# Performance work log

Measured on AMD Instinct MI355X. Metric: run time of the kernel, lower is better.

Reference implementation:

```python
import jax, jax.numpy as jnp
import numpy as np

H = 256      # hidden_dim
NH = 4       # num_heads
DK = H // NH # per-head dim
NL = 2       # num self-attn layers
TL = 6       # transformer_num_layers (output repeat)
PTS_DIM = 3


def _layer_norm(x, g, b, eps=1e-5):
    m = jnp.mean(x, axis=-1, keepdims=True)
    v = jnp.mean((x - m) ** 2, axis=-1, keepdims=True)
    return (x - m) / jnp.sqrt(v + eps) * g + b


def _mha(x, Wq, bq, Wk, bk, Wv, bv, Wo, bo, g, bb, bias):
    # x: [B,N,H]; bias: [B,NH,N,N]; way='add' (att_spm_type='add')
    B, N, _ = x.shape
    q = (x @ Wq + bq).reshape(B, N, NH, DK).transpose(0, 2, 1, 3)  # [B,h,N,d]
    k = (x @ Wk + bk).reshape(B, N, NH, DK).transpose(0, 2, 1, 3)
    v = (x @ Wv + bv).reshape(B, N, NH, DK).transpose(0, 2, 1, 3)
    att = jnp.einsum('bhnd,bhmd->bhnm', q, k) / np.sqrt(DK).astype(np.float32)
    att = jax.nn.softmax(att + bias, axis=-1)
    out = jnp.einsum('bhnm,bhmd->bhnd', att, v).transpose(0, 2, 1, 3).reshape(B, N, H)
    out = out @ Wo + bo
    return _layer_norm(x + out, g, bb)


def setup_inputs() -> dict:
    key = jax.random.key(0)
    ks = jax.random.split(key, 16)
    B, N = 1, 512
    s = 0.02  # weight init scale
    inp = {
        'history_states': jax.random.normal(ks[0], (TL, B, N, H), jnp.float32),
        'all_lanes_preds': jax.random.normal(ks[1], (TL, B, N, 33), jnp.float32),
        'fc_W': jax.random.normal(ks[2], (H, H), jnp.float32) * s,
        'fc_b': jnp.zeros((H,), jnp.float32),
        'Wq': jax.random.normal(ks[3], (NL, H, H), jnp.float32) * s,
        'bq': jnp.zeros((NL, H), jnp.float32),
        'Wk': jax.random.normal(ks[4], (NL, H, H), jnp.float32) * s,
        'bk': jnp.zeros((NL, H), jnp.float32),
        'Wv': jax.random.normal(ks[5], (NL, H, H), jnp.float32) * s,
        'bv': jnp.zeros((NL, H), jnp.float32),
        'Wo': jax.random.normal(ks[6], (NL, H, H), jnp.float32) * s,
        'bo': jnp.zeros((NL, H), jnp.float32),
        'ln_g': jnp.ones((NL, H), jnp.float32),
        'ln_b': jnp.zeros((NL, H), jnp.float32),
        'mlp1_W': jax.random.normal(ks[7], (H, H), jnp.float32) * s,
        'mlp1_b': jnp.zeros((H,), jnp.float32),
        'mlp2_W': jax.random.normal(ks[8], (H, H), jnp.float32) * s,
        'mlp2_b': jnp.zeros((H,), jnp.float32),
        'cls_W1': jax.random.normal(ks[9], (2 * H, H), jnp.float32) * s,
        'cls_b1': jnp.zeros((H,), jnp.float32),
        'cls_W2': jax.random.normal(ks[10], (H, 1), jnp.float32) * s,
        'cls_b2': jnp.zeros((1,), jnp.float32),
    }
    return inp


def reference(history_states, all_lanes_preds, fc_W, fc_b, Wq, bq, Wk, bk, Wv, bv,
              Wo, bo, ln_g, ln_b, mlp1_W, mlp1_b, mlp2_W, mlp2_b,
              cls_W1, cls_b1, cls_W2, cls_b2):
    query_feats = history_states[-1]                 # [B,N,H]
    coords = all_lanes_preds[-1]                      # [B,N,33]
    B, N, C = coords.shape
    coords = coords.reshape(B, N, C // PTS_DIM, PTS_DIM)
    query_end_point = coords[:, :, -1, :]             # [B,N,3]
    key_start_point = coords[:, :, 0, :]              # [B,N,3]

    # pairwise distance bias: dist[b,i,j] = ||key_start[j] - query_end[i]||
    diff = key_start_point[:, None, :, :] - query_end_point[:, :, None, :]
    dist = jnp.sqrt(jnp.sum(diff ** 2, axis=-1))[:, None, :, :]  # [B,1,N,N]
    dw = 1.0 / (dist + 0.01)
    dw = dw / jnp.sum(dw, axis=2, keepdims=True)      # normalize over dim 2
    zeros = jnp.zeros_like(dw)
    dist_weights = jax.lax.stop_gradient(
        jnp.concatenate([dw, -dist, zeros, zeros], axis=1))  # [B,4,N,N]

    # features_concat: Linear + ReLU
    x = jax.nn.relu(query_feats @ fc_W + fc_b)

    for i in range(NL):
        x = _mha(x, Wq[i], bq[i], Wk[i], bk[i], Wv[i], bv[i],
                 Wo[i], bo[i], ln_g[i], ln_b[i], dist_weights)

    # lclc relationship head: per-side MLP, pairwise concat, classifier
    o1 = jax.nn.relu(x @ mlp1_W + mlp1_b)             # [B,N,H]
    o2 = jax.nn.relu(x @ mlp2_W + mlp2_b)
    pair = jnp.concatenate([
        jnp.broadcast_to(o1[:, :, None, :], (B, N, N, H)),
        jnp.broadcast_to(o2[:, None, :, :], (B, N, N, H))], axis=-1)  # [B,N,N,2H]
    z = jax.nn.relu(pair @ cls_W1 + cls_b1)
    lclc = (z @ cls_W2 + cls_b2)[..., 0]              # [B,N,N]
    all_lclc_preds = jnp.broadcast_to(lclc[None], (TL, B, N, N))
    return all_lclc_preds
```

## Files before the change

### kernel.cpp

```cpp
#include <hip/hip_runtime.h>
#include <math.h>


#define NTOK 512
#define HDIM 256
#define DKH  64
#define NHEAD 4
#define TLEN 6
#define WSZ  65536
#define PSTR 520

typedef __attribute__((ext_vector_type(8))) short bf16x8;
typedef __attribute__((ext_vector_type(4))) float f32x4;

__device__ __forceinline__ ushort f2bf(float f)
{
    unsigned u = __builtin_bit_cast(unsigned, f);
    u += 0x7FFFu + ((u >> 16) & 1u);
    return (ushort)(u >> 16);
}

struct PKArg {
    const float* w[13];
    const float* qf; const float* pl;
    ushort* wpk; ushort* qf16;
    float *dist, *dwraw, *inv_cs;
};

__global__ __launch_bounds__(256) void pack_kernel(PKArg p)
{
    __shared__ __align__(16) ushort smu[64 * 72];
    const int bid = blockIdx.x;
    const int t   = threadIdx.x;

    if (bid < 208) {
        const int mat  = bid >> 4;
        const int tile = bid & 15;
        const int k0   = (tile >> 2) * 64;
        const int c0   = (tile & 3) * 64;
        const float* W = p.w[mat];
#pragma unroll
        for (int j = 0; j < 4; ++j) {
            const int i  = t + j * 256;
            const int r  = i >> 4, c4 = i & 15;
            const float4 v4 = *(const float4*)&W[(k0 + r) * HDIM + c0 + c4 * 4];
            smu[(c4 * 4 + 0) * 72 + r] = f2bf(v4.x);
            smu[(c4 * 4 + 1) * 72 + r] = f2bf(v4.y);
            smu[(c4 * 4 + 2) * 72 + r] = f2bf(v4.z);
            smu[(c4 * 4 + 3) * 72 + r] = f2bf(v4.w);
        }
        __syncthreads();
#pragma unroll
        for (int j = 0; j < 2; ++j) {
            const int i  = t + j * 256;
            const int cr = i >> 3, kk = i & 7;
            const uint4 v = *(const uint4*)&smu[cr * 72 + kk * 8];
            *(uint4*)&p.wpk[mat * WSZ + (c0 + cr) * HDIM + k0 + kk * 8] = v;
        }
    } else if (bid < 224) {
        const int r0 = (bid - 208) * 32;
#pragma unroll
        for (int j = 0; j < 8; ++j) {
            const int i  = t + j * 256;
            const int r  = i >> 6, c4 = i & 63;
            const float4 v4 = *(const float4*)&p.qf[(r0 + r) * HDIM + c4 * 4];
            ushort4 s = {f2bf(v4.x), f2bf(v4.y), f2bf(v4.z), f2bf(v4.w)};
            *(ushort4*)&p.qf16[(r0 + r) * HDIM + c4 * 4] = s;
        }
    } else {
        float* smf = (float*)smu;
        float* qe  = smf;
        float* red = smf + 1536;
        const int item = bid - 224;
        for (int i = t; i < 512; i += 256) {
            qe[i * 3 + 0] = p.pl[i * 33 + 30];
            qe[i * 3 + 1] = p.pl[i * 33 + 31];
            qe[i * 3 + 2] = p.pl[i * 33 + 32];
        }
        __syncthreads();
        const int m   = item * 64 + (t & 63);
        const int nch = t >> 6;
        const float kx = p.pl[m * 33 + 0], ky = p.pl[m * 33 + 1], kz = p.pl[m * 33 + 2];
        float cs = 0.f;
        for (int n = nch * 128; n < nch * 128 + 128; ++n) {
            const float dx = kx - qe[n * 3 + 0];
            const float dy = ky - qe[n * 3 + 1];
            const float dz = kz - qe[n * 3 + 2];
            const float dd = sqrtf(dx * dx + dy * dy + dz * dz);
            const float w  = 1.0f / (dd + 0.01f);
            p.dist[n * NTOK + m]  = dd;
            p.dwraw[n * NTOK + m] = w;
            cs += w;
        }
        red[nch * 64 + (t & 63)] = cs;
        __syncthreads();
        if (t < 64)
            p.inv_cs[item * 64 + t] =
                1.0f / (red[t] + red[64 + t] + red[128 + t] + red[192 + t]);
    }
}

struct GB { const ushort* A16; const ushort* Wt; const float* b;
            float* C; ushort* C16; ushort* C16T; };

__global__ __launch_bounds__(256) void gemm_bf(GB g0, GB g1, GB g2, int relu)
{
    const int bid = blockIdx.x;
    const GB g = (bid < 64) ? g0 : (bid < 128) ? g1 : g2;
    const int t = threadIdx.x;
    const int wv = t >> 6, lane = t & 63;
    const int gw = (bid & 63) * 4 + wv;
    const int rg = gw >> 3, cg = gw & 7;
    const int lr = lane & 15, lg = lane >> 4, lk = lg * 8;

    const ushort* Arow = g.A16 + (rg * 16 + lr) * HDIM + lk;
    const ushort* Brow = g.Wt + (cg * 32 + lr) * HDIM + lk;

    f32x4 acc[2];
    acc[0] = (f32x4){0.f, 0.f, 0.f, 0.f};
    acc[1] = (f32x4){0.f, 0.f, 0.f, 0.f};

#pragma unroll
    for (int ks = 0; ks < 8; ++ks) {
        const bf16x8 a = *(const bf16x8*)&Arow[ks * 32];
#pragma unroll
        for (int j = 0; j < 2; ++j) {
            const bf16x8 b = *(const bf16x8*)&Brow[j * 16 * HDIM + ks * 32];
            acc[j] = __builtin_amdgcn_mfma_f32_16x16x32_bf16(a, b, acc[j], 0, 0, 0);
        }
    }

    const int orow = rg * 16 + lg * 4;
#pragma unroll
    for (int j = 0; j < 2; ++j) {
        const int col = cg * 32 + j * 16 + lr;
        const float bbv = g.b ? g.b[col] : 0.f;
        float o[4];
#pragma unroll
        for (int r = 0; r < 4; ++r) {
            o[r] = acc[j][r] + bbv;
            if (relu) o[r] = fmaxf(o[r], 0.f);
            if (g.C)   g.C[(orow + r) * HDIM + col] = o[r];
            if (g.C16) g.C16[(orow + r) * HDIM + col] = f2bf(o[r]);
        }
        if (g.C16T) {
            ushort4 s = {f2bf(o[0]), f2bf(o[1]), f2bf(o[2]), f2bf(o[3])};
            *(ushort4*)&g.C16T[col * NTOK + orow] = s;
        }
    }
}

__global__ __launch_bounds__(256) void attn_fused(
    const ushort* __restrict__ q16, const ushort* __restrict__ k16,
    const ushort* __restrict__ vT16, const float* __restrict__ dist,
    const float* __restrict__ dwraw, const float* __restrict__ inv_cs,
    ushort* __restrict__ ao16)
{
    __shared__ __align__(16) ushort P_lds[16 * PSTR];
    __shared__ __align__(16) float exch[4][16][64];
    __shared__ float rmax[4][16];
    __shared__ float psums[4][16];

    const int bid = blockIdx.x;
    const int h  = bid >> 5;
    const int n0 = (bid & 31) * 16;
    const int t  = threadIdx.x;
    const int wv = t >> 6, lane = t & 63;
    const int lr = lane & 15, lg = lane >> 4, lk = lg * 8;
    const int mW = wv * 128;

    const ushort* Qrow = q16 + (n0 + lr) * HDIM + h * DKH + lk;
    const bf16x8 a0 = *(const bf16x8*)&Qrow[0];
    const bf16x8 a1 = *(const bf16x8*)&Qrow[32];

    f32x4 accs[8];
#pragma unroll
    for (int cg = 0; cg < 8; ++cg) accs[cg] = (f32x4){0.f, 0.f, 0.f, 0.f};
#pragma unroll
    for (int cg = 0; cg < 8; ++cg) {
        const ushort* Brow = k16 + (mW + cg * 16 + lr) * HDIM + h * DKH + lk;
        accs[cg] = __builtin_amdgcn_mfma_f32_16x16x32_bf16(
            a0, *(const bf16x8*)&Brow[0], accs[cg], 0, 0, 0);
        accs[cg] = __builtin_amdgcn_mfma_f32_16x16x32_bf16(
            a1, *(const bf16x8*)&Brow[32], accs[cg], 0, 0, 0);
    }

    float s[8][4];
#pragma unroll
    for (int cg = 0; cg < 8; ++cg) {
        const int m = mW + cg * 16 + lr;
        const float ic = (h == 0) ? inv_cs[m] : 0.f;
#pragma unroll
        for (int rg = 0; rg < 4; ++rg) {
            const int n = n0 + lg * 4 + rg;
            float b = 0.f;
            if (h == 0)      b = dwraw[n * NTOK + m] * ic;
            else if (h == 1) b = -dist[n * NTOK + m];
            s[cg][rg] = accs[cg][rg] * 0.125f + b;
        }
    }

    float mx[4];
#pragma unroll
    for (int rg = 0; rg < 4; ++rg) {
        float m = s[0][rg];
#pragma unroll
        for (int cg = 1; cg < 8; ++cg) m = fmaxf(m, s[cg][rg]);
#pragma unroll
        for (int o = 1; o < 16; o <<= 1) m = fmaxf(m, __shfl_xor(m, o));
        mx[rg] = m;
    }
    if (lr == 0)
#pragma unroll
        for (int rg = 0; rg < 4; ++rg) rmax[wv][lg * 4 + rg] = mx[rg];
    __syncthreads();
    float mxf[4];
#pragma unroll
    for (int rg = 0; rg < 4; ++rg) {
        const int row = lg * 4 + rg;
        mxf[rg] = fmaxf(fmaxf(rmax[0][row], rmax[1][row]),
                        fmaxf(rmax[2][row], rmax[3][row]));
    }

    float ps[4] = {0.f, 0.f, 0.f, 0.f};
#pragma unroll
    for (int cg = 0; cg < 8; ++cg)
#pragma unroll
        for (int rg = 0; rg < 4; ++rg) {
            const float e = __expf(s[cg][rg] - mxf[rg]);
            ps[rg] += e;
            P_lds[(lg * 4 + rg) * PSTR + mW + cg * 16 + lr] = f2bf(e);
        }
#pragma unroll
    for (int rg = 0; rg < 4; ++rg) {
#pragma unroll
        for (int o = 1; o < 16; o <<= 1) ps[rg] += __shfl_xor(ps[rg], o);
    }
    if (lr == 0)
#pragma unroll
        for (int rg = 0; rg < 4; ++rg) psums[wv][lg * 4 + rg] = ps[rg];
    __syncthreads();

    f32x4 acco[4];
#pragma unroll
    for (int db = 0; db < 4; ++db) acco[db] = (f32x4){0.f, 0.f, 0.f, 0.f};
#pragma unroll
    for (int c = 0; c < 4; ++c) {
        const bf16x8 pa = *(const bf16x8*)&P_lds[lr * PSTR + mW + c * 32 + lk];
#pragma unroll
        for (int db = 0; db < 4; ++db) {
            const bf16x8 b = *(const bf16x8*)
                &vT16[(h * DKH + db * 16 + lr) * NTOK + mW + c * 32 + lk];
            acco[db] = __builtin_amdgcn_mfma_f32_16x16x32_bf16(pa, b, acco[db], 0, 0, 0);
        }
    }
#pragma unroll
    for (int db = 0; db < 4; ++db)
#pragma unroll
        for (int rg = 0; rg < 4; ++rg)
            exch[wv][lg * 4 + rg][db * 16 + lr] = acco[db][rg];
    __syncthreads();

    {
        const int r = t >> 4, d4 = t & 15;
        f32x4 sum = *(const f32x4*)&exch[0][r][d4 * 4];
        sum += *(const f32x4*)&exch[1][r][d4 * 4];
        sum += *(const f32x4*)&exch[2][r][d4 * 4];
        sum += *(const f32x4*)&exch[3][r][d4 * 4];
        const float inv = 1.0f / (psums[0][r] + psums[1][r] + psums[2][r] + psums[3][r]);
        ushort4 o = {f2bf(sum.x * inv), f2bf(sum.y * inv),
                     f2bf(sum.z * inv), f2bf(sum.w * inv)};
        *(ushort4*)&ao16[(n0 + r) * HDIM + h * DKH + d4 * 4] = o;
    }
}

__global__ __launch_bounds__(256) void oprojln(
    const ushort* __restrict__ ao16, const ushort* __restrict__ WoT,
    const float* __restrict__ bo, const float* __restrict__ g,
    const float* __restrict__ bb, float* __restrict__ x,
    ushort* __restrict__ x16)
{
    __shared__ float red[4][16];

    const int n0 = blockIdx.x * 16;
    const int t  = threadIdx.x;
    const int wv = t >> 6, lane = t & 63;
    const int lr = lane & 15, lg = lane >> 4, lk = lg * 8;

    const ushort* Arow = ao16 + (n0 + lr) * HDIM + lk;

    f32x4 acc[4];
#pragma unroll
    for (int j = 0; j < 4; ++j) acc[j] = (f32x4){0.f, 0.f, 0.f, 0.f};

#pragma unroll
    for (int ks = 0; ks < 8; ++ks) {
        const bf16x8 a = *(const bf16x8*)&Arow[ks * 32];
#pragma unroll
        for (int j = 0; j < 4; ++j) {
            const bf16x8 b = *(const bf16x8*)
                &WoT[(wv * 64 + j * 16 + lr) * HDIM + ks * 32 + lk];
            acc[j] = __builtin_amdgcn_mfma_f32_16x16x32_bf16(a, b, acc[j], 0, 0, 0);
        }
    }

#pragma unroll
    for (int j = 0; j < 4; ++j) {
        const int col = wv * 64 + j * 16 + lr;
        const float bc = bo[col];
#pragma unroll
        for (int rg = 0; rg < 4; ++rg)
            acc[j][rg] += bc + x[(n0 + lg * 4 + rg) * HDIM + col];
    }

    float sm[4];
#pragma unroll
    for (int rg = 0; rg < 4; ++rg) {
        float s = 0.f;
#pragma unroll
        for (int j = 0; j < 4; ++j) s += acc[j][rg];
#pragma unroll
        for (int o = 1; o < 16; o <<= 1) s += __shfl_xor(s, o);
        sm[rg] = s;
    }
    if (lr == 0)
#pragma unroll
        for (int rg = 0; rg < 4; ++rg) red[wv][lg * 4 + rg] = sm[rg];
    __syncthreads();
    float mean[4];
#pragma unroll
    for (int rg = 0; rg < 4; ++rg) {
        const int row = lg * 4 + rg;
        mean[rg] = (red[0][row] + red[1][row] + red[2][row] + red[3][row]) * (1.f / 256.f);
    }
    __syncthreads();

#pragma unroll
    for (int rg = 0; rg < 4; ++rg) {
        float s2 = 0.f;
#pragma unroll
        for (int j = 0; j < 4; ++j) {
            const float c = acc[j][rg] - mean[rg];
            s2 += c * c;
        }
#pragma unroll
        for (int o = 1; o < 16; o <<= 1) s2 += __shfl_xor(s2, o);
        sm[rg] = s2;
    }
    if (lr == 0)
#pragma unroll
        for (int rg = 0; rg < 4; ++rg) red[wv][lg * 4 + rg] = sm[rg];
    __syncthreads();
    float rstd[4];
#pragma unroll
    for (int rg = 0; rg < 4; ++rg) {
        const int row = lg * 4 + rg;
        const float var = (red[0][row] + red[1][row] + red[2][row] + red[3][row]) * (1.f / 256.f);
        rstd[rg] = rsqrtf(var + 1e-5f);
    }

#pragma unroll
    for (int j = 0; j < 4; ++j) {
        const int col = wv * 64 + j * 16 + lr;
        const float gg = g[col], bv = bb[col];
#pragma unroll
        for (int rg = 0; rg < 4; ++rg) {
            const int row = n0 + lg * 4 + rg;
            const float o = (acc[j][rg] - mean[rg]) * rstd[rg] * gg + bv;
            x[row * HDIM + col]   = o;
            x16[row * HDIM + col] = f2bf(o);
        }
    }
}

__global__ __launch_bounds__(256) void pair_cls(const float* __restrict__ U1,
                                                const float* __restrict__ U2,
                                                const float* __restrict__ W2,
                                                const float* __restrict__ b2,
                                                float* __restrict__ out)
{
    __shared__ __align__(16) float u1s[32][260];
    __shared__ __align__(16) float u2s[32][260];
    __shared__ __align__(16) float w2s[256];
    const int t  = threadIdx.x;
    const int n0 = blockIdx.y * 32, m0 = blockIdx.x * 32;

    for (int i = t; i < 32 * 64; i += 256) {
        const int r = i >> 6, c4 = i & 63;
        *(float4*)&u1s[r][c4 * 4] = *(const float4*)&U1[(n0 + r) * HDIM + c4 * 4];
        *(float4*)&u2s[r][c4 * 4] = *(const float4*)&U2[(m0 + r) * HDIM + c4 * 4];
    }
    if (t < 64) *(float4*)&w2s[t * 4] = *(const float4*)&W2[t * 4];
    __syncthreads();

    const int tx = t & 15, ty = t >> 4;
    float acc[2][2] = {};
    for (int h4 = 0; h4 < 64; ++h4) {
        const float4 a0 = *(const float4*)&u1s[ty * 2][h4 * 4];
        const float4 a1 = *(const float4*)&u1s[ty * 2 + 1][h4 * 4];
        const float4 b0 = *(const float4*)&u2s[tx * 2][h4 * 4];
        const float4 b1 = *(const float4*)&u2s[tx * 2 + 1][h4 * 4];
        const float4 w  = *(const float4*)&w2s[h4 * 4];
#define RT(A, B) fmaxf((A) + (B), 0.f)
        acc[0][0] += RT(a0.x,b0.x)*w.x + RT(a0.y,b0.y)*w.y + RT(a0.z,b0.z)*w.z + RT(a0.w,b0.w)*w.w;
        acc[0][1] += RT(a0.x,b1.x)*w.x + RT(a0.y,b1.y)*w.y + RT(a0.z,b1.z)*w.z + RT(a0.w,b1.w)*w.w;
        acc[1][0] += RT(a1.x,b0.x)*w.x + RT(a1.y,b0.y)*w.y + RT(a1.z,b0.z)*w.z + RT(a1.w,b0.w)*w.w;
        acc[1][1] += RT(a1.x,b1.x)*w.x + RT(a1.y,b1.y)*w.y + RT(a1.z,b1.z)*w.z + RT(a1.w,b1.w)*w.w;
#undef RT
    }
    const float bbv = b2[0];
#pragma unroll
    for (int ii = 0; ii < 2; ++ii)
#pragma unroll
        for (int jj = 0; jj < 2; ++jj) {
            const float val = acc[ii][jj] + bbv;
            const int n = n0 + ty * 2 + ii;
            const int m = m0 + tx * 2 + jj;
#pragma unroll
            for (int tl = 0; tl < TLEN; ++tl)
                out[tl * NTOK * NTOK + n * NTOK + m] = val;
        }
}

extern "C" void kernel_launch(void* const* d_in, const int* in_sizes, int n_in,
                              void* d_out, int out_size, void* d_ws, size_t ws_size,
                              hipStream_t stream)
{
    const float* hs   = (const float*)d_in[0];
    const float* qf   = hs + 5 * NTOK * HDIM;
    const float* alp  = (const float*)d_in[1];
    const float* pl   = alp + 5 * NTOK * 33;
    const float* fc_W = (const float*)d_in[2];
    const float* fc_b = (const float*)d_in[3];
    const float* Wq   = (const float*)d_in[4];
    const float* bq   = (const float*)d_in[5];
    const float* Wk   = (const float*)d_in[6];
    const float* bk   = (const float*)d_in[7];
    const float* Wv   = (const float*)d_in[8];
    const float* bv   = (const float*)d_in[9];
    const float* Wo   = (const float*)d_in[10];
    const float* bo   = (const float*)d_in[11];
    const float* lng  = (const float*)d_in[12];
    const float* lnb  = (const float*)d_in[13];
    const float* m1W  = (const float*)d_in[14];
    const float* m1b  = (const float*)d_in[15];
    const float* m2W  = (const float*)d_in[16];
    const float* m2b  = (const float*)d_in[17];
    const float* cW1  = (const float*)d_in[18];
    const float* cb1  = (const float*)d_in[19];
    const float* cW2  = (const float*)d_in[20];
    const float* cb2  = (const float*)d_in[21];
    float* out = (float*)d_out;

    const int NN  = NTOK * NTOK;
    const int NH_ = NTOK * HDIM;
    float* ws     = (float*)d_ws;
    float* dist   = ws;
    float* dwraw  = ws + NN;
    float* inv_cs = ws + 2 * NN;
    float* x      = ws + 2 * NN + 512;
    float* U1     = x + NH_;
    float* U2     = U1 + NH_;
    ushort* u16   = (ushort*)(U2 + NH_);
    ushort* wpk   = u16;
    ushort* qf16  = wpk + 13 * WSZ;
    ushort* x16   = qf16 + NH_;
    ushort* q16   = x16 + NH_;
    ushort* k16   = q16 + NH_;
    ushort* vT16  = k16 + NH_;
    ushort* ao16  = vT16 + NH_;
    ushort* o116  = ao16 + NH_;
    ushort* o216  = o116 + NH_;

    PKArg pk;
    pk.w[0]  = fc_W;
    pk.w[1]  = Wq;  pk.w[2]  = Wq + WSZ;
    pk.w[3]  = Wk;  pk.w[4]  = Wk + WSZ;
    pk.w[5]  = Wv;  pk.w[6]  = Wv + WSZ;
    pk.w[7]  = Wo;  pk.w[8]  = Wo + WSZ;
    pk.w[9]  = m1W; pk.w[10] = m2W;
    pk.w[11] = cW1; pk.w[12] = cW1 + WSZ;
    pk.qf = qf; pk.pl = pl;
    pk.wpk = wpk; pk.qf16 = qf16;
    pk.dist = dist; pk.dwraw = dwraw; pk.inv_cs = inv_cs;
    pack_kernel<<<232, 256, 0, stream>>>(pk);

    const GB gzb = {nullptr, nullptr, nullptr, nullptr, nullptr, nullptr};

    gemm_bf<<<64, 256, 0, stream>>>(
        GB{qf16, wpk + 0 * WSZ, fc_b, x, x16, nullptr}, gzb, gzb, 1);

    for (int L = 0; L < 2; ++L) {
        const ushort* wq = wpk + (1 + L) * WSZ;
        const ushort* wk = wpk + (3 + L) * WSZ;
        const ushort* wv = wpk + (5 + L) * WSZ;
        const ushort* wo = wpk + (7 + L) * WSZ;

        gemm_bf<<<192, 256, 0, stream>>>(
            GB{x16, wq, bq + L * HDIM, nullptr, q16, nullptr},
            GB{x16, wk, bk + L * HDIM, nullptr, k16, nullptr},
            GB{x16, wv, bv + L * HDIM, nullptr, nullptr, vT16}, 0);

        attn_fused<<<128, 256, 0, stream>>>(
            q16, k16, vT16, dist, dwraw, inv_cs, ao16);

        oprojln<<<32, 256, 0, stream>>>(
            ao16, wo, bo + L * HDIM, lng + L * HDIM, lnb + L * HDIM, x, x16);
    }

    gemm_bf<<<128, 256, 0, stream>>>(
        GB{x16, wpk + 9 * WSZ, m1b, nullptr, o116, nullptr},
        GB{x16, wpk + 10 * WSZ, m2b, nullptr, o216, nullptr}, gzb, 1);
    gemm_bf<<<128, 256, 0, stream>>>(
        GB{o116, wpk + 11 * WSZ, cb1, U1, nullptr, nullptr},
        GB{o216, wpk + 12 * WSZ, nullptr, U2, nullptr, nullptr}, gzb, 0);

    pair_cls<<<dim3(16, 16), 256, 0, stream>>>(U1, U2, cW2, cb2, out);
}
```

Baseline: 109.7 us.

## Fuse row-slab GEMM chains into fewer kernels with LDS-resident panels

Replaces the separate generic GEMM launches with fused per-16-row-slab kernels. These chain fc→QKV, oproj+LayerNorm→next-layer QKV, and oproj+LN→MLP1/MLP2→classifier-W1, keeping the intermediate activations in LDS panels. The fc input is now converted to bf16 inside the GEMM, so the separate conversion pass in the pack kernel goes away. Kernel launches drop from 10 to 7 and several global round-trips are removed. In exchange only 32 blocks run each fused GEMM stage, and each wave does more serial MFMA work, so parallelism per stage is lower.

Measured after the change: 153.2 us. +39.6%, slower.

```diff
diff --git a/kernel.cpp b/kernel.cpp
--- a/kernel.cpp
+++ b/kernel.cpp
@@ -9,6 +9,7 @@
 #define TLEN 6
 #define WSZ  65536
 #define PSTR 520
+#define XPS  264
 
 typedef __attribute__((ext_vector_type(8))) short bf16x8;
 typedef __attribute__((ext_vector_type(4))) float f32x4;
@@ -22,8 +23,8 @@
 
 struct PKArg {
     const float* w[13];
-    const float* qf; const float* pl;
-    ushort* wpk; ushort* qf16;
+    const float* pl;
+    ushort* wpk;
     float *dist, *dwraw, *inv_cs;
 };
 
@@ -57,21 +58,11 @@
             const uint4 v = *(const uint4*)&smu[cr * 72 + kk * 8];
             *(uint4*)&p.wpk[mat * WSZ + (c0 + cr) * HDIM + k0 + kk * 8] = v;
         }
-    } else if (bid < 224) {
-        const int r0 = (bid - 208) * 32;
-#pragma unroll
-        for (int j = 0; j < 8; ++j) {
-            const int i  = t + j * 256;
-            const int r  = i >> 6, c4 = i & 63;
-            const float4 v4 = *(const float4*)&p.qf[(r0 + r) * HDIM + c4 * 4];
-            ushort4 s = {f2bf(v4.x), f2bf(v4.y), f2bf(v4.z), f2bf(v4.w)};
-            *(ushort4*)&p.qf16[(r0 + r) * HDIM + c4 * 4] = s;
-        }
     } else {
         float* smf = (float*)smu;
         float* qe  = smf;
         float* red = smf + 1536;
-        const int item = bid - 224;
+        const int item = bid - 208;
         for (int i = t; i < 512; i += 256) {
             qe[i * 3 + 0] = p.pl[i * 33 + 30];
             qe[i * 3 + 1] = p.pl[i * 33 + 31];
@@ -100,54 +91,101 @@
     }
 }
 
-struct GB { const ushort* A16; const ushort* Wt; const float* b;
-            float* C; ushort* C16; ushort* C16T; };
-
-__global__ __launch_bounds__(256) void gemm_bf(GB g0, GB g1, GB g2, int relu)
-{
-    const int bid = blockIdx.x;
-    const GB g = (bid < 64) ? g0 : (bid < 128) ? g1 : g2;
+__device__ __forceinline__ void qkv_phase(
+    const ushort* __restrict__ xpan,
+    const ushort* __restrict__ WqT, const float* __restrict__ bq,
+    const ushort* __restrict__ WkT, const float* __restrict__ bk,
+    const ushort* __restrict__ WvT, const float* __restrict__ bv,
+    int slab, int c0, int lr, int lg, int lk,
+    ushort* __restrict__ q16, ushort* __restrict__ k16,
+    ushort* __restrict__ vT16)
+{
+    const ushort* Ap = xpan + lr * XPS + lk;
+#pragma unroll
+    for (int p = 0; p < 3; ++p) {
+        const ushort* Wt = (p == 0) ? WqT : (p == 1) ? WkT : WvT;
+        const float*  bb = (p == 0) ? bq  : (p == 1) ? bk  : bv;
+        f32x4 acc[4];
+#pragma unroll
+        for (int j = 0; j < 4; ++j) acc[j] = (f32x4){0.f, 0.f, 0.f, 0.f};
+#pragma unroll
+        for (int ks = 0; ks < 8; ++ks) {
+            const bf16x8 a = *(const bf16x8*)&Ap[ks * 32];
+#pragma unroll
+            for (int j = 0; j < 4; ++j) {
+                const bf16x8 b = *(const bf16x8*)&Wt[(c0 + j * 16 + lr) * HDIM + ks * 32 + lk];
+                acc[j] = __builtin_amdgcn_mfma_f32_16x16x32_bf16(a, b, acc[j], 0, 0, 0);
+            }
+        }
+#pragma unroll
+        for (int j = 0; j < 4; ++j) {
+            const int col = c0 + j * 16 + lr;
+            const float bv2 = bb[col];
+            if (p < 2) {
+                ushort* dst = (p == 0) ? q16 : k16;
+#pragma unroll
+                for (int rg = 0; rg < 4; ++rg)
+                    dst[(slab + lg * 4 + rg) * HDIM + col] = f2bf(acc[j][rg] + bv2);
+            } else {
+                ushort4 s = {f2bf(acc[j][0] + bv2), f2bf(acc[j][1] + bv2),
+                             f2bf(acc[j][2] + bv2), f2bf(acc[j][3] + bv2)};
+                *(ushort4*)&vT16[col * NTOK + slab + lg * 4] = s;
+            }
+        }
+    }
+}
+
+__global__ __launch_bounds__(256) void fcqkv(
+    const float* __restrict__ qf, const ushort* __restrict__ fcWt,
+    const float* __restrict__ fcb,
+    const ushort* __restrict__ WqT, const float* __restrict__ bq,
+    const ushort* __restrict__ WkT, const float* __restrict__ bk,
+    const ushort* __restrict__ WvT, const float* __restrict__ bv,
+    float* __restrict__ x, ushort* __restrict__ q16,
+    ushort* __restrict__ k16, ushort* __restrict__ vT16)
+{
+    __shared__ __align__(16) ushort xpan[16 * XPS];
+    const int slab = blockIdx.x * 16;
     const int t = threadIdx.x;
     const int wv = t >> 6, lane = t & 63;
-    const int gw = (bid & 63) * 4 + wv;
-    const int rg = gw >> 3, cg = gw & 7;
     const int lr = lane & 15, lg = lane >> 4, lk = lg * 8;
-
-    const ushort* Arow = g.A16 + (rg * 16 + lr) * HDIM + lk;
-    const ushort* Brow = g.Wt + (cg * 32 + lr) * HDIM + lk;
-
-    f32x4 acc[2];
-    acc[0] = (f32x4){0.f, 0.f, 0.f, 0.f};
-    acc[1] = (f32x4){0.f, 0.f, 0.f, 0.f};
-
-#pragma unroll
-    for (int ks = 0; ks < 8; ++ks) {
-        const bf16x8 a = *(const bf16x8*)&Arow[ks * 32];
-#pragma unroll
-        for (int j = 0; j < 2; ++j) {
-            const bf16x8 b = *(const bf16x8*)&Brow[j * 16 * HDIM + ks * 32];
-            acc[j] = __builtin_amdgcn_mfma_f32_16x16x32_bf16(a, b, acc[j], 0, 0, 0);
-        }
-    }
-
-    const int orow = rg * 16 + lg * 4;
-#pragma unroll
-    for (int j = 0; j < 2; ++j) {
-        const int col = cg * 32 + j * 16 + lr;
-        const float bbv = g.b ? g.b[col] : 0.f;
-        float o[4];
-#pragma unroll
-        for (int r = 0; r < 4; ++r) {
-            o[r] = acc[j][r] + bbv;
-            if (relu) o[r] = fmaxf(o[r], 0.f);
-            if (g.C)   g.C[(orow + r) * HDIM + col] = o[r];
-            if (g.C16) g.C16[(orow + r) * HDIM + col] = f2bf(o[r]);
-        }
-        if (g.C16T) {
-            ushort4 s = {f2bf(o[0]), f2bf(o[1]), f2bf(o[2]), f2bf(o[3])};
-            *(ushort4*)&g.C16T[col * NTOK + orow] = s;
-        }
-    }
+    const int c0 = wv * 64;
+
+    {
+        f32x4 acc[4];
+#pragma unroll
+        for (int j = 0; j < 4; ++j) acc[j] = (f32x4){0.f, 0.f, 0.f, 0.f};
+        const float* Aq = qf + (slab + lr) * HDIM + lk;
+#pragma unroll
+        for (int ks = 0; ks < 8; ++ks) {
+            const float4 a0 = *(const float4*)&Aq[ks * 32];
+            const float4 a1 = *(const float4*)&Aq[ks * 32 + 4];
+            bf16x8 a;
+            a[0] = (short)f2bf(a0.x); a[1] = (short)f2bf(a0.y);
+            a[2] = (short)f2bf(a0.z); a[3] = (short)f2bf(a0.w);
+            a[4] = (short)f2bf(a1.x); a[5] = (short)f2bf(a1.y);
+            a[6] = (short)f2bf(a1.z); a[7] = (short)f2bf(a1.w);
+#pragma unroll
+            for (int j = 0; j < 4; ++j) {
+                const bf16x8 b = *(const bf16x8*)&fcWt[(c0 + j * 16 + lr) * HDIM + ks * 32 + lk];
+                acc[j] = __builtin_amdgcn_mfma_f32_16x16x32_bf16(a, b, acc[j], 0, 0, 0);
+            }
+        }
+#pragma unroll
+        for (int j = 0; j < 4; ++j) {
+            const int col = c0 + j * 16 + lr;
+            const float bbv = fcb[col];
+#pragma unroll
+            for (int rg = 0; rg < 4; ++rg) {
+                const float o = fmaxf(acc[j][rg] + bbv, 0.f);
+                x[(slab + lg * 4 + rg) * HDIM + col] = o;
+                xpan[(lg * 4 + rg) * XPS + col] = f2bf(o);
+            }
+        }
+    }
+    __syncthreads();
+    qkv_phase(xpan, WqT, bq, WkT, bk, WvT, bv, slab, c0, lr, lg, lk,
+              q16, k16, vT16);
 }
 
 __global__ __launch_bounds__(256) void attn_fused(
@@ -274,43 +312,32 @@
     }
 }
 
-__global__ __launch_bounds__(256) void oprojln(
+__device__ __forceinline__ void oprojln_phase(
     const ushort* __restrict__ ao16, const ushort* __restrict__ WoT,
-    const float* __restrict__ bo, const float* __restrict__ g,
-    const float* __restrict__ bb, float* __restrict__ x,
-    ushort* __restrict__ x16)
-{
-    __shared__ float red[4][16];
-
-    const int n0 = blockIdx.x * 16;
-    const int t  = threadIdx.x;
-    const int wv = t >> 6, lane = t & 63;
-    const int lr = lane & 15, lg = lane >> 4, lk = lg * 8;
-
-    const ushort* Arow = ao16 + (n0 + lr) * HDIM + lk;
-
-    f32x4 acc[4];
+    const float* __restrict__ bo, const float* __restrict__ gamma,
+    const float* __restrict__ beta, const float* __restrict__ x,
+    int slab, int c0, int wv, int lr, int lg, int lk,
+    float red[4][16], f32x4 acc[4])
+{
+    const ushort* Arow = ao16 + (slab + lr) * HDIM + lk;
 #pragma unroll
     for (int j = 0; j < 4; ++j) acc[j] = (f32x4){0.f, 0.f, 0.f, 0.f};
-
 #pragma unroll
     for (int ks = 0; ks < 8; ++ks) {
         const bf16x8 a = *(const bf16x8*)&Arow[ks * 32];
 #pragma unroll
         for (int j = 0; j < 4; ++j) {
-            const bf16x8 b = *(const bf16x8*)
-                &WoT[(wv * 64 + j * 16 + lr) * HDIM + ks * 32 + lk];
+            const bf16x8 b = *(const bf16x8*)&WoT[(c0 + j * 16 + lr) * HDIM + ks * 32 + lk];
             acc[j] = __builtin_amdgcn_mfma_f32_16x16x32_bf16(a, b, acc[j], 0, 0, 0);
         }
     }
-
 #pragma unroll
     for (int j = 0; j < 4; ++j) {
-        const int col = wv * 64 + j * 16 + lr;
+        const int col = c0 + j * 16 + lr;
         const float bc = bo[col];
 #pragma unroll
         for (int rg = 0; rg < 4; ++rg)
-            acc[j][rg] += bc + x[(n0 + lg * 4 + rg) * HDIM + col];
+            acc[j][rg] += bc + x[(slab + lg * 4 + rg) * HDIM + col];
     }
 
     float sm[4];
@@ -358,17 +385,135 @@
         const float var = (red[0][row] + red[1][row] + red[2][row] + red[3][row]) * (1.f / 256.f);
         rstd[rg] = rsqrtf(var + 1e-5f);
     }
-
 #pragma unroll
     for (int j = 0; j < 4; ++j) {
-        const int col = wv * 64 + j * 16 + lr;
-        const float gg = g[col], bv = bb[col];
+        const int col = c0 + j * 16 + lr;
+        const float gg = gamma[col], bv = beta[col];
+#pragma unroll
+        for (int rg = 0; rg < 4; ++rg)
+            acc[j][rg] = (acc[j][rg] - mean[rg]) * rstd[rg] * gg + bv;
+    }
+}
+
+__global__ __launch_bounds__(256) void oprojqkv(
+    const ushort* __restrict__ ao16, const ushort* __restrict__ WoT,
+    const float* __restrict__ bo, const float* __restrict__ gamma,
+    const float* __restrict__ beta,
+    const ushort* __restrict__ WqT, const float* __restrict__ bq,
+    const ushort* __restrict__ WkT, const float* __restrict__ bk,
+    const ushort* __restrict__ WvT, const float* __restrict__ bv,
+    float* __restrict__ x, ushort* __restrict__ q16,
+    ushort* __restrict__ k16, ushort* __restrict__ vT16)
+{
+    __shared__ __align__(16) ushort xpan[16 * XPS];
+    __shared__ float red[4][16];
+    const int slab = blockIdx.x * 16;
+    const int t = threadIdx.x;
+    const int wv = t >> 6, lane = t & 63;
+    const int lr = lane & 15, lg = lane >> 4, lk = lg * 8;
+    const int c0 = wv * 64;
+
+    f32x4 acc[4];
+    oprojln_phase(ao16, WoT, bo, gamma, beta, x, slab, c0, wv, lr, lg, lk, red, acc);
+#pragma unroll
+    for (int j = 0; j < 4; ++j) {
+        const int col = c0 + j * 16 + lr;
 #pragma unroll
         for (int rg = 0; rg < 4; ++rg) {
-            const int row = n0 + lg * 4 + rg;
-            const float o = (acc[j][rg] - mean[rg]) * rstd[rg] * gg + bv;
-            x[row * HDIM + col]   = o;
-            x16[row * HDIM + col] = f2bf(o);
+            x[(slab + lg * 4 + rg) * HDIM + col] = acc[j][rg];
+            xpan[(lg * 4 + rg) * XPS + col] = f2bf(acc[j][rg]);
+        }
+    }
+    __syncthreads();
+    qkv_phase(xpan, WqT, bq, WkT, bk, WvT, bv, slab, c0, lr, lg, lk,
+              q16, k16, vT16);
+}
+
+__global__ __launch_bounds__(256) void oprojmlpU(
+    const ushort* __restrict__ ao16, const ushort* __restrict__ WoT,
+    const float* __restrict__ bo, const float* __restrict__ gamma,
+    const float* __restrict__ beta,
+    const ushort* __restrict__ m1WT, const float* __restrict__ m1b,
+    const ushort* __restrict__ m2WT, const float* __restrict__ m2b,
+    const ushort* __restrict__ cW1aT, const float* __restrict__ cb1,
+    const ushort* __restrict__ cW1bT,
+    const float* __restrict__ x, float* __restrict__ U1, float* __restrict__ U2)
+{
+    __shared__ __align__(16) ushort xpan[16 * XPS];
+    __shared__ __align__(16) ushort o1pan[16 * XPS];
+    __shared__ __align__(16) ushort o2pan[16 * XPS];
+    __shared__ float red[4][16];
+    const int slab = blockIdx.x * 16;
+    const int t = threadIdx.x;
+    const int wv = t >> 6, lane = t & 63;
+    const int lr = lane & 15, lg = lane >> 4, lk = lg * 8;
+    const int c0 = wv * 64;
+
+    f32x4 acc[4];
+    oprojln_phase(ao16, WoT, bo, gamma, beta, x, slab, c0, wv, lr, lg, lk, red, acc);
+#pragma unroll
+    for (int j = 0; j < 4; ++j) {
+        const int col = c0 + j * 16 + lr;
+#pragma unroll
+        for (int rg = 0; rg < 4; ++rg)
+            xpan[(lg * 4 + rg) * XPS + col] = f2bf(acc[j][rg]);
+    }
+    __syncthreads();
+
+    const ushort* Ap = xpan + lr * XPS + lk;
+#pragma unroll
+    for (int p = 0; p < 2; ++p) {
+        const ushort* Wt = p ? m2WT : m1WT;
+        const float*  bb = p ? m2b  : m1b;
+        ushort* opan     = p ? o2pan : o1pan;
+        f32x4 a2[4];
+#pragma unroll
+        for (int j = 0; j < 4; ++j) a2[j] = (f32x4){0.f, 0.f, 0.f, 0.f};
+#pragma unroll
+        for (int ks = 0; ks < 8; ++ks) {
+            const bf16x8 a = *(const bf16x8*)&Ap[ks * 32];
+#pragma unroll
+            for (int j = 0; j < 4; ++j) {
+                const bf16x8 b = *(const bf16x8*)&Wt[(c0 + j * 16 + lr) * HDIM + ks * 32 + lk];
+                a2[j] = __builtin_amdgcn_mfma_f32_16x16x32_bf16(a, b, a2[j], 0, 0, 0);
+            }
+        }
+#pragma unroll
+        for (int j = 0; j < 4; ++j) {
+            const int col = c0 + j * 16 + lr;
+            const float bbv = bb[col];
+#pragma unroll
+            for (int rg = 0; rg < 4; ++rg)
+                opan[(lg * 4 + rg) * XPS + col] = f2bf(fmaxf(a2[j][rg] + bbv, 0.f));
+        }
+    }
+    __syncthreads();
+
+#pragma unroll
+    for (int p = 0; p < 2; ++p) {
+        const ushort* opan = p ? o2pan : o1pan;
+        const ushort* Wt   = p ? cW1bT : cW1aT;
+        float* U           = p ? U2 : U1;
+        const ushort* Ao = opan + lr * XPS + lk;
+        f32x4 a2[4];
+#pragma unroll
+        for (int j = 0; j < 4; ++j) a2[j] = (f32x4){0.f, 0.f, 0.f, 0.f};
+#pragma unroll
+        for (int ks = 0; ks < 8; ++ks) {
+            const bf16x8 a = *(const bf16x8*)&Ao[ks * 32];
+#pragma unroll
+            for (int j = 0; j < 4; ++j) {
+                const bf16x8 b = *(const bf16x8*)&Wt[(c0 + j * 16 + lr) * HDIM + ks * 32 + lk];
+                a2[j] = __builtin_amdgcn_mfma_f32_16x16x32_bf16(a, b, a2[j], 0, 0, 0);
+            }
+        }
+#pragma unroll
+        for (int j = 0; j < 4; ++j) {
+            const int col = c0 + j * 16 + lr;
+            const float bbv = (p == 0) ? cb1[col] : 0.f;
+#pragma unroll
+            for (int rg = 0; rg < 4; ++rg)
+                U[(slab + lg * 4 + rg) * HDIM + col] = a2[j][rg] + bbv;
         }
     }
 }
@@ -463,14 +608,10 @@
     float* U2     = U1 + NH_;
     ushort* u16   = (ushort*)(U2 + NH_);
     ushort* wpk   = u16;
-    ushort* qf16  = wpk + 13 * WSZ;
-    ushort* x16   = qf16 + NH_;
-    ushort* q16   = x16 + NH_;
+    ushort* q16   = wpk + 13 * WSZ;
     ushort* k16   = q16 + NH_;
     ushort* vT16  = k16 + NH_;
     ushort* ao16  = vT16 + NH_;
-    ushort* o116  = ao16 + NH_;
-    ushort* o216  = o116 + NH_;
 
     PKArg pk;
     pk.w[0]  = fc_W;
@@ -480,40 +621,31 @@
     pk.w[7]  = Wo;  pk.w[8]  = Wo + WSZ;
     pk.w[9]  = m1W; pk.w[10] = m2W;
     pk.w[11] = cW1; pk.w[12] = cW1 + WSZ;
-    pk.qf = qf; pk.pl = pl;
-    pk.wpk = wpk; pk.qf16 = qf16;
+    pk.pl = pl;
+    pk.wpk = wpk;
     pk.dist = dist; pk.dwraw = dwraw; pk.inv_cs = inv_cs;
-    pack_kernel<<<232, 256, 0, stream>>>(pk);
-
-    const GB gzb = {nullptr, nullptr, nullptr, nullptr, nullptr, nullptr};
-
-    gemm_bf<<<64, 256, 0, stream>>>(
-        GB{qf16, wpk + 0 * WSZ, fc_b, x, x16, nullptr}, gzb, gzb, 1);
-
-    for (int L = 0; L < 2; ++L) {
-        const ushort* wq = wpk + (1 + L) * WSZ;
-        const ushort* wk = wpk + (3 + L) * WSZ;
-        const ushort* wv = wpk + (5 + L) * WSZ;
-        const ushort* wo = wpk + (7 + L) * WSZ;
-
-        gemm_bf<<<192, 256, 0, stream>>>(
-            GB{x16, wq, bq + L * HDIM, nullptr, q16, nullptr},
-            GB{x16, wk, bk + L * HDIM, nullptr, k16, nullptr},
-            GB{x16, wv, bv + L * HDIM, nullptr, nullptr, vT16}, 0);
-
-        attn_fused<<<128, 256, 0, stream>>>(
-            q16, k16, vT16, dist, dwraw, inv_cs, ao16);
-
-        oprojln<<<32, 256, 0, stream>>>(
-            ao16, wo, bo + L * HDIM, lng + L * HDIM, lnb + L * HDIM, x, x16);
-    }
-
-    gemm_bf<<<128, 256, 0, stream>>>(
-        GB{x16, wpk + 9 * WSZ, m1b, nullptr, o116, nullptr},
-        GB{x16, wpk + 10 * WSZ, m2b, nullptr, o216, nullptr}, gzb, 1);
-    gemm_bf<<<128, 256, 0, stream>>>(
-        GB{o116, wpk + 11 * WSZ, cb1, U1, nullptr, nullptr},
-        GB{o216, wpk + 12 * WSZ, nullptr, U2, nullptr, nullptr}, gzb, 0);
+    pack_kernel<<<216, 256, 0, stream>>>(pk);
+
+    fcqkv<<<32, 256, 0, stream>>>(
+        qf, wpk + 0 * WSZ, fc_b,
+        wpk + 1 * WSZ, bq, wpk + 3 * WSZ, bk, wpk + 5 * WSZ, bv,
+        x, q16, k16, vT16);
+
+    attn_fused<<<128, 256, 0, stream>>>(q16, k16, vT16, dist, dwraw, inv_cs, ao16);
+
+    oprojqkv<<<32, 256, 0, stream>>>(
+        ao16, wpk + 7 * WSZ, bo, lng, lnb,
+        wpk + 2 * WSZ, bq + HDIM, wpk + 4 * WSZ, bk + HDIM,
+        wpk + 6 * WSZ, bv + HDIM,
+        x, q16, k16, vT16);
+
+    attn_fused<<<128, 256, 0, stream>>>(q16, k16, vT16, dist, dwraw, inv_cs, ao16);
+
+    oprojmlpU<<<32, 256, 0, stream>>>(
+        ao16, wpk + 8 * WSZ, bo + HDIM, lng + HDIM, lnb + HDIM,
+        wpk + 9 * WSZ, m1b, wpk + 10 * WSZ, m2b,
+        wpk + 11 * WSZ, cb1, wpk + 12 * WSZ,
+        x, U1, U2);
 
     pair_cls<<<dim3(16, 16), 256, 0, stream>>>(U1, U2, cW2, cb2, out);
 }
```
